# Kernel optimization log

Hardware: AMD Instinct MI355X
Metric: run time of the kernel (lower is better)

Reference implementation:

```python
import jax, jax.numpy as jnp
import numpy as np

K = 3          # conv kernel size
STRIDE = 1     # conv stride (SAME padding)
ITERS = 3      # DR routing iterations
EPS = 1e-9     # squash epsilon


def squash(s, axis):
    # v = ||s||^2 / (1 + ||s||^2) * s / ||s||   (DR squash)
    sq = jnp.sum(s * s, axis=axis, keepdims=True)
    return (sq / (1.0 + sq)) * s * jax.lax.rsqrt(sq + EPS)


def setup_inputs() -> dict:
    key = jax.random.key(0)
    k1, k2, k3 = jax.random.split(key, 3)
    b, h, w, iCaps, iPose = 8, 12, 12, 32, 16
    oCaps, oPose = 32, 16
    x = jax.random.normal(k1, (b, h, w, iCaps, iPose), dtype=jnp.float32)
    # Wa: [kk*iCaps, oCaps, iPose, oPose] (leading 1 of the TF weight is dropped)
    fan = K * K * iCaps * iPose
    W = jax.random.normal(k2, (K * K * iCaps, oCaps, iPose, oPose), dtype=jnp.float32) * np.float32(np.sqrt(2.0 / fan))
    # biases: [oCaps, oPose] (TF shape [1,1,oCaps,oPose,1], broadcastable)
    biases = jax.random.normal(k3, (oCaps, oPose), dtype=jnp.float32) * 0.05
    return {"x": x, "W": W, "biases": biases}


def _kernel_tile(x2d):
    # im2col for SAME padding, stride 1.  x2d: (b, h, w, C) -> (b, h, w, k*k, C)
    b, h, w, C = x2d.shape
    pad = K // 2
    xp = jnp.pad(x2d, ((0, 0), (pad, pad), (pad, pad), (0, 0)))
    patches = jnp.stack(
        [xp[:, i:i + h, j:j + w, :] for i in range(K) for j in range(K)], axis=3
    )
    return patches  # (b, h, w, k*k, C)


def reference(x, W, biases):
    b, h, w, iCaps, iPose = x.shape
    iC = K * K * iCaps
    oC, oP = biases.shape

    # 1. kernel_tile: gather k*k neighborhoods
    patches = _kernel_tile(x.reshape(b, h, w, iCaps * iPose))      # (b,h,w,kk,iCaps*iPose)
    u = patches.reshape(b * h * w, iC, iPose)                       # (bx, iC, iPose)

    # 2. transform_view (vector capsules): votes[n,i,c,:] = u[n,i,:] @ W[i,c,:,:]
    votes = jnp.einsum('nip,icpq->nicq', u, W)                      # (bx, iC, oC, oP)

    # 3. DR routing
    bx = votes.shape[0]
    logits = jnp.zeros((bx, iC, oC), dtype=votes.dtype)
    v = None
    for ii in range(ITERS):
        c = jax.nn.softmax(logits, axis=2)                          # coupling coeffs over oCaps
        s = jnp.einsum('nic,nicq->ncq', c, votes) + biases          # (bx, oC, oP)
        v = squash(s, axis=2)
        if ii < ITERS - 1:
            logits = logits + jnp.einsum('nicq,ncq->nic', votes, v)  # agreement

    return v.reshape(b, h, w, oC, oP)
```

## Files before the change

kernel.cpp:

```cpp
#include <hip/hip_runtime.h>
#include <stdint.h>

typedef unsigned short ushort_t;

#define KK3 3
#define IC 32
#define IP 16
#define OC 32
#define OP 16
#define NI 288
#define HH 12
#define WWW 12
#define NTOT 1152
#define CQ 512
#define EPSQ 1e-9f
#define RWAVES 4
#define RSTEPS 36
#define NIP 144
#define NIG 18
#define IPG 8
#define SROW 132
#define SPAR (16 * SROW)
#define SWAVE (2 * SPAR)

typedef __attribute__((ext_vector_type(8))) short bf16x8;
typedef __attribute__((ext_vector_type(4))) float f32x4;

__device__ __forceinline__ float bf_lo(unsigned u) { return __uint_as_float(u << 16); }
__device__ __forceinline__ float bf_hi(unsigned u) { return __uint_as_float(u & 0xffff0000u); }
__device__ __forceinline__ ushort_t f2bf(float f) {
    unsigned u = __float_as_uint(f);
    return (ushort_t)((u + 0x7fffu + ((u >> 16) & 1u)) >> 16);
}

__global__ __launch_bounds__(64) void pack_kernel(
    const float* __restrict__ W, ushort_t* __restrict__ Wp)
{
    const int blk = blockIdx.x;
    const int ip = blk >> 5;
    const int c = blk & 31;
    const int l = threadIdx.x;
    const int i = ip * 2 + ((l >> 5) & 1);
    const int p0 = ((l >> 4) & 1) * 8;
    const int q = l & 15;
    const float* src = W + (((size_t)(i * 32 + c) * 16 + p0) * 16 + q);
    union { ushort_t s[8]; uint4 u4; } o;
#pragma unroll
    for (int j = 0; j < 8; ++j) o.s[j] = f2bf(src[(size_t)j * 16]);
    *(uint4*)(Wp + ((size_t)blk * 64 + l) * 8) = o.u4;
}

__global__ __launch_bounds__(256) void votes_s0_kernel(
    const float* __restrict__ x, const ushort_t* __restrict__ Wp,
    ushort_t* __restrict__ votes, float* __restrict__ s0_part,
    int nStart, int nCount)
{
    __shared__ ushort_t slab[4 * SWAVE];

    const int t = threadIdx.x;
    const int w = t >> 6;
    const int l = t & 63;
    const int pxt = blockIdx.x;
    const int ig = blockIdx.y;

    const int n = nStart + pxt * 16 + (l & 15);
    const int b = n / (HH * WWW);
    const int rem = n % (HH * WWW);
    const int y = rem / WWW;
    const int xx = rem % WWW;
    const int ioff = (l >> 5) & 1;
    const int p0 = ((l >> 4) & 1) * 8;

    const int q = l & 15;
    const int r0 = (l >> 4) * 4;
    const int j16 = l & 15;
    const int g4 = l >> 4;

    ushort_t* const myslab = slab + w * SWAVE;

    const bf16x8 z8 = {0, 0, 0, 0, 0, 0, 0, 0};
    const f32x4 z4 = {0.f, 0.f, 0.f, 0.f};

    f32x4 accs0[8];
#pragma unroll
    for (int ctl = 0; ctl < 8; ++ctl) accs0[ctl] = z4;

    for (int m = 0; m < IPG; ++m) {
        const int ip = ig * IPG + m;
        union { ushort_t s[8]; bf16x8 v; } ua;
        {
            const int i = ip * 2 + ioff;
            const int ky = i / (KK3 * IC);
            const int kx = (i / IC) % KK3;
            const int ic = i & (IC - 1);
            const int sy = y + ky - 1;
            const int sx = xx + kx - 1;
            if (sy >= 0 && sy < HH && sx >= 0 && sx < WWW) {
                const float* s = x + ((((size_t)b * HH + sy) * WWW + sx) * IC + ic) * IP + p0;
                const float4 v0 = *(const float4*)s;
                const float4 v1 = *(const float4*)(s + 4);
                ua.s[0] = f2bf(v0.x); ua.s[1] = f2bf(v0.y); ua.s[2] = f2bf(v0.z); ua.s[3] = f2bf(v0.w);
                ua.s[4] = f2bf(v1.x); ua.s[5] = f2bf(v1.y); ua.s[6] = f2bf(v1.z); ua.s[7] = f2bf(v1.w);
            } else {
#pragma unroll
                for (int j = 0; j < 8; ++j) ua.s[j] = 0;
            }
        }

#pragma unroll
        for (int ctl = 0; ctl < 8; ++ctl) {
            const int ct = w * 8 + ctl;
            const bf16x8 frag = *(const bf16x8*)(Wp + (((size_t)ip * 32 + ct) * 64 + l) * 8);
            const bf16x8 be = (l < 32) ? frag : z8;
            const bf16x8 bo = (l < 32) ? z8 : frag;
            const f32x4 ve = __builtin_amdgcn_mfma_f32_16x16x32_bf16(ua.v, be, z4, 0, 0, 0);
            const f32x4 vo = __builtin_amdgcn_mfma_f32_16x16x32_bf16(ua.v, bo, z4, 0, 0, 0);
            accs0[ctl] = __builtin_amdgcn_mfma_f32_16x16x32_bf16(ua.v, frag, accs0[ctl], 0, 0, 0);
#pragma unroll
            for (int r = 0; r < 4; ++r) {
                myslab[(r0 + r) * SROW + ctl * 16 + q] = f2bf(ve[r]);
                myslab[SPAR + (r0 + r) * SROW + ctl * 16 + q] = f2bf(vo[r]);
            }
        }

#pragma unroll
        for (int s = 0; s < 2; ++s) {
#pragma unroll
            for (int h = 0; h < 4; ++h) {
                const int row = h * 4 + g4;
                const ushort_t* sp = myslab + s * SPAR + row * SROW + j16 * 8;
                const uint2 lo = *(const uint2*)sp;
                const uint2 hi = *(const uint2*)(sp + 4);
                ushort_t* dst = votes + ((size_t)(pxt * 16 + row) * NI + (2 * ip + s)) * CQ
                                + w * 128 + j16 * 8;
                uint4 o; o.x = lo.x; o.y = lo.y; o.z = hi.x; o.w = hi.y;
                *(uint4*)dst = o;
            }
        }
    }

    {
#pragma unroll
        for (int ctl = 0; ctl < 8; ++ctl) {
            const int cq = (w * 8 + ctl) * 16 + q;
#pragma unroll
            for (int r = 0; r < 4; ++r)
                s0_part[((size_t)ig * nCount + pxt * 16 + r0 + r) * CQ + cq] = accs0[ctl][r];
        }
    }
}

#define UNPACK16(A, B)                                                     \
    const float f0 = bf_lo(A.x), f1 = bf_hi(A.x), f2 = bf_lo(A.y),         \
                f3 = bf_hi(A.y), f4 = bf_lo(A.z), f5 = bf_hi(A.z),         \
                f6 = bf_lo(A.w), f7 = bf_hi(A.w), f8 = bf_lo(B.x),         \
                f9 = bf_hi(B.x), f10 = bf_lo(B.y), f11 = bf_hi(B.y),       \
                f12 = bf_lo(B.z), f13 = bf_hi(B.z), f14 = bf_lo(B.w),      \
                f15 = bf_hi(B.w);

__global__ __launch_bounds__(256) void route_kernel(
    const ushort_t* __restrict__ votes, const float* __restrict__ s0_part,
    const float* __restrict__ bias, float* __restrict__ out,
    int nStart, int nCount)
{
    __shared__ float lg_lds[NI * OC];
    __shared__ float sPart[RWAVES][CQ];
    __shared__ float s_sh[CQ];
    __shared__ float v_sh[CQ];
    __shared__ float fac_sh[OC];

    const int bn = blockIdx.x;
    const int t = threadIdx.x;
    const int wv = t >> 6;
    const int l = t & 63;
    const int isub = l >> 5;
    const int c = l & 31;
    const int iBase = 2 * wv + isub;

    const ushort_t* pbase = votes + (size_t)bn * NI * CQ + (size_t)iBase * CQ + c * OP;
    const size_t stepB = (size_t)8 * CQ;

#pragma unroll
    for (int rep = 0; rep < 2; ++rep) {
        const int k = t + rep * 256;
        float s = 0.f;
#pragma unroll
        for (int g = 0; g < NIG; ++g)
            s += s0_part[((size_t)g * nCount + bn) * CQ + k];
        s_sh[k] = fmaf(s, 1.0f / OC, bias[k]);
    }
    __syncthreads();
    if (t < OC) {
        float sq = 0.f;
#pragma unroll
        for (int q = 0; q < OP; ++q) { const float s = s_sh[t * OP + q]; sq = fmaf(s, s, sq); }
        fac_sh[t] = (sq / (1.0f + sq)) * rsqrtf(sq + EPSQ);
    }
    __syncthreads();
#pragma unroll
    for (int rep = 0; rep < 2; ++rep) {
        const int k = t + rep * 256;
        v_sh[k] = s_sh[k] * fac_sh[k >> 4];
    }
    __syncthreads();

    float sa[16];
    float vr[16];

#define RBODY(AA, BB, rr)                                                   \
        {                                                                   \
            UNPACK16(AA, BB)                                                \
            float a = f0 * vr[0];                                           \
            a = fmaf(f1, vr[1], a);   a = fmaf(f2, vr[2], a);               \
            a = fmaf(f3, vr[3], a);   a = fmaf(f4, vr[4], a);               \
            a = fmaf(f5, vr[5], a);   a = fmaf(f6, vr[6], a);               \
            a = fmaf(f7, vr[7], a);   a = fmaf(f8, vr[8], a);               \
            a = fmaf(f9, vr[9], a);   a = fmaf(f10, vr[10], a);             \
            a = fmaf(f11, vr[11], a); a = fmaf(f12, vr[12], a);             \
            a = fmaf(f13, vr[13], a); a = fmaf(f14, vr[14], a);             \
            a = fmaf(f15, vr[15], a);                                       \
            const int li = (iBase + 8 * (rr)) * OC + c;                     \
            if (it == 0) lg_lds[li] = a;                                    \
            else          a += lg_lds[li];                                  \
            const float e = __expf(a);                                      \
            float es = e;                                                   \
            es += __shfl_xor(es, 1);                                        \
            es += __shfl_xor(es, 2);                                        \
            es += __shfl_xor(es, 4);                                        \
            es += __shfl_xor(es, 8);                                        \
            es += __shfl_xor(es, 16);                                       \
            const float coup = __fdividef(e, es);                           \
            sa[0] = fmaf(coup, f0, sa[0]);   sa[1] = fmaf(coup, f1, sa[1]); \
            sa[2] = fmaf(coup, f2, sa[2]);   sa[3] = fmaf(coup, f3, sa[3]); \
            sa[4] = fmaf(coup, f4, sa[4]);   sa[5] = fmaf(coup, f5, sa[5]); \
            sa[6] = fmaf(coup, f6, sa[6]);   sa[7] = fmaf(coup, f7, sa[7]); \
            sa[8] = fmaf(coup, f8, sa[8]);   sa[9] = fmaf(coup, f9, sa[9]); \
            sa[10] = fmaf(coup, f10, sa[10]); sa[11] = fmaf(coup, f11, sa[11]); \
            sa[12] = fmaf(coup, f12, sa[12]); sa[13] = fmaf(coup, f13, sa[13]); \
            sa[14] = fmaf(coup, f14, sa[14]); sa[15] = fmaf(coup, f15, sa[15]); \
        }
#define RPREF(AA, BB, rn)                                                   \
        if ((rn) < RSTEPS) {                                                \
            const uint4* pn = (const uint4*)(pbase + (size_t)(rn) * stepB); \
            AA = pn[0]; BB = pn[1];                                         \
        }

#pragma unroll
    for (int it = 0; it < 2; ++it) {
#pragma unroll
        for (int k = 0; k < 4; ++k) {
            const float4 v4 = *(const float4*)&v_sh[c * 16 + 4 * k];
            vr[4*k] = v4.x; vr[4*k+1] = v4.y; vr[4*k+2] = v4.z; vr[4*k+3] = v4.w;
        }
#pragma unroll
        for (int q = 0; q < 16; ++q) sa[q] = 0.f;

        uint4 A0, B0, A1, B1, A2, B2, A3, B3, A4, B4, A5, B5;
        RPREF(A0, B0, 0)
        RPREF(A1, B1, 1)
        RPREF(A2, B2, 2)
        RPREF(A3, B3, 3)
        RPREF(A4, B4, 4)
        RPREF(A5, B5, 5)
        for (int r = 0; r < RSTEPS; r += 6) {
            RBODY(A0, B0, r)     RPREF(A0, B0, r + 6)
            RBODY(A1, B1, r + 1) RPREF(A1, B1, r + 7)
            RBODY(A2, B2, r + 2) RPREF(A2, B2, r + 8)
            RBODY(A3, B3, r + 3) RPREF(A3, B3, r + 9)
            RBODY(A4, B4, r + 4) RPREF(A4, B4, r + 10)
            RBODY(A5, B5, r + 5) RPREF(A5, B5, r + 11)
        }

#pragma unroll
        for (int q = 0; q < 16; ++q) sa[q] += __shfl_xor(sa[q], 32);
        if (isub == 0) {
#pragma unroll
            for (int k = 0; k < 4; ++k)
                *(float4*)&sPart[wv][c * 16 + 4 * k] = make_float4(sa[4*k], sa[4*k+1], sa[4*k+2], sa[4*k+3]);
        }
        __syncthreads();
#pragma unroll
        for (int rep = 0; rep < 2; ++rep) {
            const int k = t + rep * 256;
            float s = (sPart[0][k] + sPart[1][k]) + (sPart[2][k] + sPart[3][k]);
            s_sh[k] = s + bias[k];
        }
        __syncthreads();
        if (t < OC) {
            float sq = 0.f;
#pragma unroll
            for (int q = 0; q < OP; ++q) { const float s = s_sh[t * OP + q]; sq = fmaf(s, s, sq); }
            fac_sh[t] = (sq / (1.0f + sq)) * rsqrtf(sq + EPSQ);
        }
        __syncthreads();
#pragma unroll
        for (int rep = 0; rep < 2; ++rep) {
            const int k = t + rep * 256;
            v_sh[k] = s_sh[k] * fac_sh[k >> 4];
        }
        __syncthreads();
    }

#pragma unroll
    for (int rep = 0; rep < 2; ++rep) {
        const int k = t + rep * 256;
        out[(size_t)(nStart + bn) * CQ + k] = v_sh[k];
    }
}

extern "C" void kernel_launch(void* const* d_in, const int* in_sizes, int n_in,
                              void* d_out, int out_size, void* d_ws, size_t ws_size,
                              hipStream_t stream)
{
    const float* x = (const float*)d_in[0];
    const float* Wg = (const float*)d_in[1];
    const float* bias = (const float*)d_in[2];
    float* out = (float*)d_out;

    const size_t perN = (size_t)NI * CQ * sizeof(ushort_t);
    const size_t packBytes = (size_t)NIP * 32 * 64 * 8 * 2;
    const size_t perNpart = (size_t)NIG * CQ * sizeof(float);

    int chunk = 768;
    if (ws_size < (size_t)chunk * (perN + perNpart) + packBytes) {
        size_t avail = (ws_size > packBytes) ? ws_size - packBytes : 0;
        chunk = (int)(avail / (perN + perNpart));
        chunk &= ~15;
        if (chunk < 16) chunk = 16;
    }
    const size_t packOff = (size_t)chunk * perN;
    const size_t partOff = packOff + packBytes;

    ushort_t* votes = (ushort_t*)d_ws;
    ushort_t* Wp = (ushort_t*)((char*)d_ws + packOff);
    float* s0_part = (float*)((char*)d_ws + partOff);

    hipLaunchKernelGGL(pack_kernel, dim3(NIP * 32), dim3(64), 0, stream, Wg, Wp);

    for (int start = 0; start < NTOT; start += chunk) {
        const int cnt = (NTOT - start < chunk) ? (NTOT - start) : chunk;
        hipLaunchKernelGGL(votes_s0_kernel, dim3(cnt / 16, NIG), dim3(256), 0, stream,
                           x, Wp, votes, s0_part, start, cnt);
        hipLaunchKernelGGL(route_kernel, dim3(cnt), dim3(256), 0, stream,
                           votes, s0_part, bias, out, start, cnt);
    }
}
```

Before: 249.3 us.

## Replace stored routing logits with accumulated output vector via linearity

Uses the linearity of the agreement logits in v (logits = votes·(v0+v1)) to drop the per-block LDS logit array. The second routing pass now dots each vote with the running sum of v vectors instead of reading and writing stored logits. A dummy padded LDS array of similar size is added, apparently to keep the per-block shared-memory footprint and therefore occupancy unchanged, so the only effect should be removing the LDS traffic. It also writes the final output straight from s and the squash factor, dropping one LDS round trip and a barrier.

New measurement: 246.4 us. No clear change (-1.1%).

```diff
diff --git a/kernel.cpp b/kernel.cpp
--- a/kernel.cpp
+++ b/kernel.cpp
@@ -163,14 +163,16 @@
     const float* __restrict__ bias, float* __restrict__ out,
     int nStart, int nCount)
 {
-    __shared__ float lg_lds[NI * OC];
     __shared__ float sPart[RWAVES][CQ];
     __shared__ float s_sh[CQ];
-    __shared__ float v_sh[CQ];
+    __shared__ float vcur_sh[CQ];
     __shared__ float fac_sh[OC];
+    __shared__ float pad_lds[5632];
 
     const int bn = blockIdx.x;
     const int t = threadIdx.x;
+    ((volatile float*)pad_lds)[t] = 0.f;
+
     const int wv = t >> 6;
     const int l = t & 63;
     const int isub = l >> 5;
@@ -200,14 +202,14 @@
 #pragma unroll
     for (int rep = 0; rep < 2; ++rep) {
         const int k = t + rep * 256;
-        v_sh[k] = s_sh[k] * fac_sh[k >> 4];
+        vcur_sh[k] = s_sh[k] * fac_sh[k >> 4];
     }
     __syncthreads();
 
     float sa[16];
     float vr[16];
 
-#define RBODY(AA, BB, rr)                                                   \
+#define RBODY(AA, BB)                                                       \
         {                                                                   \
             UNPACK16(AA, BB)                                                \
             float a = f0 * vr[0];                                           \
@@ -219,9 +221,6 @@
             a = fmaf(f11, vr[11], a); a = fmaf(f12, vr[12], a);             \
             a = fmaf(f13, vr[13], a); a = fmaf(f14, vr[14], a);             \
             a = fmaf(f15, vr[15], a);                                       \
-            const int li = (iBase + 8 * (rr)) * OC + c;                     \
-            if (it == 0) lg_lds[li] = a;                                    \
-            else          a += lg_lds[li];                                  \
             const float e = __expf(a);                                      \
             float es = e;                                                   \
             es += __shfl_xor(es, 1);                                        \
@@ -249,7 +248,7 @@
     for (int it = 0; it < 2; ++it) {
 #pragma unroll
         for (int k = 0; k < 4; ++k) {
-            const float4 v4 = *(const float4*)&v_sh[c * 16 + 4 * k];
+            const float4 v4 = *(const float4*)&vcur_sh[c * 16 + 4 * k];
             vr[4*k] = v4.x; vr[4*k+1] = v4.y; vr[4*k+2] = v4.z; vr[4*k+3] = v4.w;
         }
 #pragma unroll
@@ -263,12 +262,12 @@
         RPREF(A4, B4, 4)
         RPREF(A5, B5, 5)
         for (int r = 0; r < RSTEPS; r += 6) {
-            RBODY(A0, B0, r)     RPREF(A0, B0, r + 6)
-            RBODY(A1, B1, r + 1) RPREF(A1, B1, r + 7)
-            RBODY(A2, B2, r + 2) RPREF(A2, B2, r + 8)
-            RBODY(A3, B3, r + 3) RPREF(A3, B3, r + 9)
-            RBODY(A4, B4, r + 4) RPREF(A4, B4, r + 10)
-            RBODY(A5, B5, r + 5) RPREF(A5, B5, r + 11)
+            RBODY(A0, B0) RPREF(A0, B0, r + 6)
+            RBODY(A1, B1) RPREF(A1, B1, r + 7)
+            RBODY(A2, B2) RPREF(A2, B2, r + 8)
+            RBODY(A3, B3) RPREF(A3, B3, r + 9)
+            RBODY(A4, B4) RPREF(A4, B4, r + 10)
+            RBODY(A5, B5) RPREF(A5, B5, r + 11)
         }
 
 #pragma unroll
@@ -293,18 +292,20 @@
             fac_sh[t] = (sq / (1.0f + sq)) * rsqrtf(sq + EPSQ);
         }
         __syncthreads();
-#pragma unroll
-        for (int rep = 0; rep < 2; ++rep) {
-            const int k = t + rep * 256;
-            v_sh[k] = s_sh[k] * fac_sh[k >> 4];
-        }
-        __syncthreads();
-    }
-
-#pragma unroll
-    for (int rep = 0; rep < 2; ++rep) {
-        const int k = t + rep * 256;
-        out[(size_t)(nStart + bn) * CQ + k] = v_sh[k];
+        if (it == 0) {
+#pragma unroll
+            for (int rep = 0; rep < 2; ++rep) {
+                const int k = t + rep * 256;
+                vcur_sh[k] += s_sh[k] * fac_sh[k >> 4];
+            }
+            __syncthreads();
+        } else {
+#pragma unroll
+            for (int rep = 0; rep < 2; ++rep) {
+                const int k = t + rep * 256;
+                out[(size_t)(nStart + bn) * CQ + k] = s_sh[k] * fac_sh[k >> 4];
+            }
+        }
     }
 }
 
```
